# Kernel optimization log

Measured on AMD Instinct MI355X. Metric: run time of the kernel, lower is better.

Reference implementation:

```python
import jax, jax.numpy as jnp
import numpy as np

ROPE_THETA = 500000.0


def apply_rope(x, position_ids):
    # x: (B, H, S, hd), position_ids: (B, S)
    hd = x.shape[-1]
    inv_freq = 1.0 / (ROPE_THETA ** (jnp.arange(0, hd, 2, dtype=x.dtype) / hd))  # (hd/2,)
    freqs = position_ids.astype(x.dtype)[:, :, None] * inv_freq  # (B, S, hd/2)
    sin = jnp.sin(freqs)[:, None, :, :]  # (B, 1, S, hd/2)
    cos = jnp.cos(freqs)[:, None, :, :]
    x1 = x[..., ::2]
    x2 = x[..., 1::2]
    even = x1 * cos - x2 * sin
    odd = x2 * cos + x1 * sin
    # interleave even/odd back: stack on a new trailing axis then flatten
    return jnp.stack([even, odd], axis=-1).reshape(x.shape)


def setup_inputs() -> dict:
    key = jax.random.key(0)
    k_x, k_q, k_k, k_v, k_o = jax.random.split(key, 5)
    B, S, D = 2, 2048, 2048
    H, H_kv = 32, 8
    hd = D // H
    x = jax.random.normal(k_x, (B, S, D), dtype=jnp.float32)
    position_ids = jnp.broadcast_to(jnp.arange(S, dtype=jnp.int64)[None, :], (B, S))
    scale = 0.02
    Wq = jax.random.normal(k_q, (D, H * hd), dtype=jnp.float32) * scale
    Wk = jax.random.normal(k_k, (D, H_kv * hd), dtype=jnp.float32) * scale
    Wv = jax.random.normal(k_v, (D, H_kv * hd), dtype=jnp.float32) * scale
    Wo = jax.random.normal(k_o, (D, D), dtype=jnp.float32) * scale
    return {"x": x, "position_ids": position_ids, "Wq": Wq, "Wk": Wk, "Wv": Wv, "Wo": Wo}


def reference(x, position_ids, Wq, Wk, Wv, Wo):
    B, S, D = x.shape
    H, H_kv = 32, 8
    hd = D // H
    G = H // H_kv  # query heads per kv head

    q = (x @ Wq).reshape(B, S, H, hd).transpose(0, 2, 1, 3)        # (B, H, S, hd)
    k = (x @ Wk).reshape(B, S, H_kv, hd).transpose(0, 2, 1, 3)     # (B, H_kv, S, hd)
    v = (x @ Wv).reshape(B, S, H_kv, hd).transpose(0, 2, 1, 3)

    q = apply_rope(q, position_ids)
    k = apply_rope(k, position_ids)

    # GQA: group query heads (B, H_kv, G, S, hd); repeat_interleave maps head h -> kv head h // G
    qg = q.reshape(B, H_kv, G, S, hd)
    scores = jnp.einsum("bkgsh,bkth->bkgst", qg, k) / jnp.sqrt(jnp.asarray(hd, x.dtype))

    causal = jnp.triu(jnp.ones((S, S), dtype=bool), 1)  # True = masked
    scores = jnp.where(causal, jnp.asarray(-jnp.inf, scores.dtype), scores)

    attn = jax.nn.softmax(scores, axis=-1)  # (B, H_kv, G, S, S)
    z = jnp.einsum("bkgst,bkth->bkgsh", attn, v)  # (B, H_kv, G, S, hd)
    z = z.reshape(B, H, S, hd).transpose(0, 2, 1, 3).reshape(B, S, D)
    return z @ Wo
```

## Files before the change

kernel.cpp:

```cpp
#include <hip/hip_runtime.h>
#include <hip/hip_bf16.h>


#define S_LEN 2048
#define DIM   2048
#define NH    32
#define NKV   8
#define HD    64
#define BS    4096
#define NQKV  3072
#define LL(x) ((long long)(x))

typedef __bf16 bf16x8 __attribute__((ext_vector_type(8)));
typedef float  f32x4  __attribute__((ext_vector_type(4)));
typedef float  f32x16 __attribute__((ext_vector_type(16)));
typedef unsigned u32x4 __attribute__((ext_vector_type(4)));

__device__ __forceinline__ unsigned short bfb(float f) {
  __hip_bfloat16 h = __float2bfloat16(f);
  return *reinterpret_cast<unsigned short*>(&h);
}

__device__ __forceinline__ unsigned cvtpk(float lo, float hi) {
  unsigned u;
  asm("v_cvt_pk_bf16_f32 %0, %1, %2" : "=v"(u) : "v"(lo), "v"(hi));
  return u;
}

__device__ __forceinline__ void gload16(const void* g, void* l) {
  __builtin_amdgcn_global_load_lds(
      (const __attribute__((address_space(1))) void*)g,
      (__attribute__((address_space(3))) void*)l, 16, 0, 0);
}

__device__ __forceinline__ void tcast_body(
    const float* __restrict__ in, unsigned short* __restrict__ out,
    int K, int N, int bx, int by, int tid, float* tile ) {
  int n0 = bx * 32, k0 = by * 32;
  int tx = tid & 31, ty = tid >> 5;
#pragma unroll
  for (int r = 0; r < 32; r += 8)
    tile[(ty + r) * 33 + tx] = in[LL(k0 + ty + r) * N + n0 + tx];
  __syncthreads();
#pragma unroll
  for (int r = 0; r < 32; r += 8)
    out[LL(n0 + ty + r) * K + k0 + tx] = bfb(tile[tx * 33 + ty + r]);
}

__global__ __launch_bounds__(256) void k_prep(
    const float* __restrict__ x,  const float* __restrict__ Wq,
    const float* __restrict__ Wk, const float* __restrict__ Wv,
    const float* __restrict__ Wo, float* __restrict__ tab,
    unsigned short* __restrict__ xb, unsigned short* __restrict__ wqkvt,
    unsigned short* __restrict__ wot) {
  __shared__ float tile[32 * 33];
  int blk = blockIdx.x, tid = threadIdx.x;
  if (blk < 256) {
    int i = blk * 256 + tid;
    int s = i >> 5, f = i & 31;
    double inv = pow(500000.0, -2.0 * (double)f / 64.0);
    double fr = (double)s * inv;
    tab[2 * i]     = (float)cos(fr);
    tab[2 * i + 1] = (float)sin(fr);
  } else if (blk < 8448) {
    int i = (blk - 256) * 256 + tid;
    float4 v = ((const float4*)x)[i];
    ushort4 o;
    o.x = bfb(v.x); o.y = bfb(v.y); o.z = bfb(v.z); o.w = bfb(v.w);
    ((ushort4*)xb)[i] = o;
  } else if (blk < 12544) {
    int t2 = blk - 8448;
    tcast_body(Wq, wqkvt, DIM, DIM, t2 & 63, t2 >> 6, tid, tile);
  } else if (blk < 13568) {
    int t3 = blk - 12544;
    tcast_body(Wk, wqkvt + LL(2048) * DIM, DIM, 512, t3 & 15, t3 >> 4, tid, tile);
  } else if (blk < 14592) {
    int t4 = blk - 13568;
    tcast_body(Wv, wqkvt + LL(2560) * DIM, DIM, 512, t4 & 15, t4 >> 4, tid, tile);
  } else {
    int t5 = blk - 14592;
    tcast_body(Wo, wot, DIM, DIM, t5 & 63, t5 >> 6, tid, tile);
  }
}

template <int MODE>
__global__ __launch_bounds__(256, 2) void k_gemm(
    const unsigned short* __restrict__ A, const unsigned short* __restrict__ Bt,
    void* __restrict__ Cout, int M, int N, int K,
    const float* __restrict__ tab, unsigned short* __restrict__ qbuf,
    unsigned short* __restrict__ kbuf, unsigned short* __restrict__ vtb) {
  __shared__ __align__(16) unsigned short As[128 * 64];
  __shared__ __align__(16) unsigned short Bs[128 * 64];
  int t = threadIdx.x;
  int lane = t & 63, w = t >> 6;
  int wr = w >> 1, wc = w & 1;
  int g = lane >> 4, r = lane & 15;
  int sw = (r & 7) * 8;
  int gx = gridDim.x;
  int nwg = gx * gridDim.y;
  int lin = blockIdx.y * gx + blockIdx.x;
  int cpx = nwg >> 3;
  int swz = (lin & 7) * cpx + (lin >> 3);
  int bx = swz % gx, by = swz / gx;
  long long rowBase = LL(by) * 128;
  long long colBase = LL(bx) * 128;

  f32x4 acc[4][4] = {};

  int c0 = t, c1 = t + 256, c2 = t + 512, c3 = t + 768;
#define SRCP(P, base, c) ((P) + ((base) + ((c) >> 3)) * K \
                               + ((((c) & 7) ^ (((c) >> 3) & 7)) * 8))
  const unsigned short* ag0 = SRCP(A, rowBase, c0);
  const unsigned short* ag1 = SRCP(A, rowBase, c1);
  const unsigned short* ag2 = SRCP(A, rowBase, c2);
  const unsigned short* ag3 = SRCP(A, rowBase, c3);
  const unsigned short* bg0 = SRCP(Bt, colBase, c0);
  const unsigned short* bg1 = SRCP(Bt, colBase, c1);
  const unsigned short* bg2 = SRCP(Bt, colBase, c2);
  const unsigned short* bg3 = SRCP(Bt, colBase, c3);
#undef SRCP
  char* lA0 = (char*)As + c0 * 16; char* lA1 = (char*)As + c1 * 16;
  char* lA2 = (char*)As + c2 * 16; char* lA3 = (char*)As + c3 * 16;
  char* lB0 = (char*)Bs + c0 * 16; char* lB1 = (char*)Bs + c1 * 16;
  char* lB2 = (char*)Bs + c2 * 16; char* lB3 = (char*)Bs + c3 * 16;

  for (int kt = 0; kt < K; kt += 64) {
    __syncthreads();
    gload16(ag0 + kt, lA0);
    gload16(ag1 + kt, lA1);
    gload16(ag2 + kt, lA2);
    gload16(ag3 + kt, lA3);
    gload16(bg0 + kt, lB0);
    gload16(bg1 + kt, lB1);
    gload16(bg2 + kt, lB2);
    gload16(bg3 + kt, lB3);
    __syncthreads();

#pragma unroll
    for (int kd = 0; kd < 2; kd++) {
      bf16x8 af[4], bfr[4];
#pragma unroll
      for (int m = 0; m < 4; m++)
        af[m] = *(const bf16x8*)(const void*)(
            As + (wr * 64 + m * 16 + r) * 64 + ((kd * 32 + g * 8) ^ sw));
#pragma unroll
      for (int n = 0; n < 4; n++)
        bfr[n] = *(const bf16x8*)(const void*)(
            Bs + (wc * 64 + n * 16 + r) * 64 + ((kd * 32 + g * 8) ^ sw));
#pragma unroll
      for (int m = 0; m < 4; m++)
#pragma unroll
        for (int n = 0; n < 4; n++)
          acc[m][n] = __builtin_amdgcn_mfma_f32_16x16x32_bf16(af[m], bfr[n], acc[m][n], 0, 0, 0);
    }
  }

  if (MODE == 0) {
#pragma unroll
    for (int m = 0; m < 4; m++)
#pragma unroll
      for (int n = 0; n < 4; n++) {
        long long row0 = rowBase + wr * 64 + m * 16 + g * 4;
        long long col = colBase + wc * 64 + n * 16 + r;
#pragma unroll
        for (int j = 0; j < 4; j++)
          ((float*)Cout)[(row0 + j) * N + col] = acc[m][n][j];
      }
  } else {
#pragma unroll
    for (int n = 0; n < 4; n++) {
      int gc0 = (int)colBase + wc * 64 + n * 16;
      int gc = gc0 + r;
      if (gc0 < 2560) {
        unsigned short* dst; int dcol, dstride; float scale;
        if (gc0 < 2048) { dst = qbuf; dcol = gc;        dstride = DIM; scale = 0.18033688f; }
        else            { dst = kbuf; dcol = gc - 2048; dstride = 512; scale = 1.0f; }
        int f = (gc & 63) >> 1;
        float sgn = (gc & 1) ? 1.f : -1.f;
#pragma unroll
        for (int m = 0; m < 4; m++) {
          long long row0 = rowBase + wr * 64 + m * 16 + g * 4;
#pragma unroll
          for (int j = 0; j < 4; j++) {
            float v = acc[m][n][j];
            float part = __shfl_xor(v, 1);
            int s = (int)((row0 + j) & (S_LEN - 1));
            float cc = tab[(s * 32 + f) * 2], ss = tab[(s * 32 + f) * 2 + 1];
            float o = (v * cc + sgn * part * ss) * scale;
            dst[(row0 + j) * dstride + dcol] = bfb(o);
          }
        }
      } else {
        int dcol = gc - 2560;
#pragma unroll
        for (int m = 0; m < 4; m++) {
          long long row0 = rowBase + wr * 64 + m * 16 + g * 4;
#pragma unroll
          for (int j = 0; j < 4; j++) {
            long long row = row0 + j;
            long long bq = row >> 11;
            int s = (int)(row & (S_LEN - 1));
            vtb[(bq * 512 + dcol) * S_LEN + s] = bfb(acc[m][n][j]);
          }
        }
      }
    }
  }
}

__global__ __launch_bounds__(256, 2) void k_attn(
    const unsigned short* __restrict__ qb, const unsigned short* __restrict__ kb,
    const unsigned short* __restrict__ vt, unsigned short* __restrict__ zb) {
  int lin = blockIdx.x + 16 * (blockIdx.y + 32 * blockIdx.z);
  int kvh = lin & 7;
  int idx = lin >> 3;
  int st = 15 - (idx >> 3);
  int b = (idx >> 2) & 1;
  int h = kvh * 4 + (idx & 3);
  int bh = b * NKV + kvh;

  int t = threadIdx.x, lane = t & 63, w = t >> 6;
  int l31 = lane & 31, hi = lane >> 5;
  int sw = (l31 & 7) * 8;

  __shared__ __align__(16) unsigned short Ks[2][64 * 64];
  __shared__ __align__(16) unsigned short Vs[2][64 * 64];

  int c0 = t, c1 = t + 256;
  const unsigned short* kg0 = kb + LL(b) * S_LEN * 512 + (c0 >> 3) * 512 + kvh * HD
                                 + (((c0 & 7) ^ ((c0 >> 3) & 7)) * 8);
  const unsigned short* kg1 = kb + LL(b) * S_LEN * 512 + (c1 >> 3) * 512 + kvh * HD
                                 + (((c1 & 7) ^ ((c1 >> 3) & 7)) * 8);
  const unsigned short* vg0 = vt + (LL(bh) * HD + (c0 >> 3)) * S_LEN
                                 + (((c0 & 7) ^ ((c0 >> 3) & 7)) * 8);
  const unsigned short* vg1 = vt + (LL(bh) * HD + (c1 >> 3)) * S_LEN
                                 + (((c1 & 7) ^ ((c1 >> 3) & 7)) * 8);

#define STAGE(bufi, kst_)                                              \
  {                                                                    \
    gload16(kg0 + LL(kst_) * 512, (char*)Ks[bufi] + c0 * 16);          \
    gload16(kg1 + LL(kst_) * 512, (char*)Ks[bufi] + c1 * 16);          \
    gload16(vg0 + (kst_), (char*)Vs[bufi] + c0 * 16);                  \
    gload16(vg1 + (kst_), (char*)Vs[bufi] + c1 * 16);                  \
  }

  int rowb = st * 128 + w * 32;
  int qg = rowb + l31;
  long long qrow = LL(b) * S_LEN + qg;

  bf16x8 qf[4];
#pragma unroll
  for (int s = 0; s < 4; s++)
    qf[s] = *(const bf16x8*)(const void*)(qb + qrow * DIM + h * HD + s * 16 + hi * 8);

  f32x16 acc0 = {}, acc1 = {};
  float mrun = -1e30f, lrun = 0.f;

  int nt = 2 * st + 2;
  STAGE(0, 0);
  for (int tt = 0; tt < nt; tt++) {
    int kst = tt * 64;
    int cur = tt & 1;
    asm volatile("s_waitcnt vmcnt(0)" ::: "memory");
    __builtin_amdgcn_s_barrier();
    __builtin_amdgcn_sched_barrier(0);
    if (tt + 1 < nt) STAGE(cur ^ 1, kst + 64);

    if (kst <= rowb + 31) {
      const unsigned short* Kc = Ks[cur];
      const unsigned short* Vc = Vs[cur];

      bf16x8 kf[2][4];
#pragma unroll
      for (int kbi = 0; kbi < 2; kbi++)
#pragma unroll
        for (int s = 0; s < 4; s++)
          kf[kbi][s] = *(const bf16x8*)(const void*)(
              Kc + (kbi * 32 + l31) * 64 + ((s * 16 + hi * 8) ^ sw));

      __builtin_amdgcn_s_setprio(1);
      f32x16 sc0 = {}, sc1 = {};
#pragma unroll
      for (int s = 0; s < 4; s++) {
        sc0 = __builtin_amdgcn_mfma_f32_32x32x16_bf16(kf[0][s], qf[s], sc0, 0, 0, 0);
        sc1 = __builtin_amdgcn_mfma_f32_32x32x16_bf16(kf[1][s], qf[s], sc1, 0, 0, 0);
      }
      __builtin_amdgcn_s_setprio(0);

      bf16x8 vf[8];
#pragma unroll
      for (int db = 0; db < 2; db++)
#pragma unroll
        for (int f = 0; f < 4; f++)
          vf[db * 4 + f] = *(const bf16x8*)(const void*)(
              Vc + (db * 32 + l31) * 64 + ((f * 16 + hi * 8) ^ sw));

      if (kst + 63 > rowb) {
#pragma unroll
        for (int q = 0; q < 16; q++) {
          int kl = (q & 3) + 8 * (q >> 2) + 4 * hi;
          if (kst + kl > qg) sc0[q] = -1e30f;
          if (kst + 32 + kl > qg) sc1[q] = -1e30f;
        }
      }

      float pm = -1e30f;
#pragma unroll
      for (int q = 0; q < 16; q++) {
        pm = fmaxf(pm, sc0[q]);
        pm = fmaxf(pm, sc1[q]);
      }
      pm = fmaxf(pm, __shfl_xor(pm, 32));
      if (__any(pm > mrun + 12.0f)) {
        float mnew = fmaxf(mrun, pm);
        float al = exp2f(mrun - mnew);
        mrun = mnew;
        lrun *= al;
        acc0 *= al;
        acc1 *= al;
      }
      f32x16 pv0, pv1;
      float ls = 0.f;
#pragma unroll
      for (int q = 0; q < 16; q++) {
        pv0[q] = exp2f(sc0[q] - mrun);
        pv1[q] = exp2f(sc1[q] - mrun);
        ls += pv0[q] + pv1[q];
      }
      lrun += ls + __shfl_xor(ls, 32);

      bf16x8 pfr[4];
#pragma unroll
      for (int f = 0; f < 4; f++) {
        int qb_ = (f & 1) * 8;
        float e0, e1, e2, e3, e4, e5, e6, e7;
        if (f < 2) {
          e0 = pv0[qb_ + 0]; e1 = pv0[qb_ + 1]; e2 = pv0[qb_ + 2]; e3 = pv0[qb_ + 3];
          e4 = pv0[qb_ + 4]; e5 = pv0[qb_ + 5]; e6 = pv0[qb_ + 6]; e7 = pv0[qb_ + 7];
        } else {
          e0 = pv1[qb_ + 0]; e1 = pv1[qb_ + 1]; e2 = pv1[qb_ + 2]; e3 = pv1[qb_ + 3];
          e4 = pv1[qb_ + 4]; e5 = pv1[qb_ + 5]; e6 = pv1[qb_ + 6]; e7 = pv1[qb_ + 7];
        }
        unsigned a0 = cvtpk(e0, e1), a1 = cvtpk(e2, e3);
        unsigned b0 = cvtpk(e4, e5), b1 = cvtpk(e6, e7);
        asm volatile("v_permlane32_swap_b32 %0, %1" : "+v"(a0), "+v"(b0));
        asm volatile("v_permlane32_swap_b32 %0, %1" : "+v"(a1), "+v"(b1));
        u32x4 uu;
        uu[0] = a0;
        uu[1] = a1;
        uu[2] = b0;
        uu[3] = b1;
        pfr[f] = *(bf16x8*)&uu;
      }

      __builtin_amdgcn_s_setprio(1);
#pragma unroll
      for (int f = 0; f < 4; f++) {
        acc0 = __builtin_amdgcn_mfma_f32_32x32x16_bf16(vf[f],     pfr[f], acc0, 0, 0, 0);
        acc1 = __builtin_amdgcn_mfma_f32_32x32x16_bf16(vf[4 + f], pfr[f], acc1, 0, 0, 0);
      }
      __builtin_amdgcn_s_setprio(0);
    }
  }

  float invl = 1.0f / lrun;
#pragma unroll
  for (int q4 = 0; q4 < 4; q4++) {
    uint2 u;
    u.x = cvtpk(acc0[q4 * 4 + 0] * invl, acc0[q4 * 4 + 1] * invl);
    u.y = cvtpk(acc0[q4 * 4 + 2] * invl, acc0[q4 * 4 + 3] * invl);
    *(uint2*)(void*)(zb + qrow * DIM + h * HD + 8 * q4 + 4 * hi) = u;
    uint2 v;
    v.x = cvtpk(acc1[q4 * 4 + 0] * invl, acc1[q4 * 4 + 1] * invl);
    v.y = cvtpk(acc1[q4 * 4 + 2] * invl, acc1[q4 * 4 + 3] * invl);
    *(uint2*)(void*)(zb + qrow * DIM + h * HD + 32 + 8 * q4 + 4 * hi) = v;
  }
#undef STAGE
}

extern "C" void kernel_launch(void* const* d_in, const int* in_sizes, int n_in,
                              void* d_out, int out_size, void* d_ws, size_t ws_size,
                              hipStream_t stream) {
  const float* x  = (const float*)d_in[0];
  const float* Wq = (const float*)d_in[2];
  const float* Wk = (const float*)d_in[3];
  const float* Wv = (const float*)d_in[4];
  const float* Wo = (const float*)d_in[5];
  float* out = (float*)d_out;

  char* wsb = (char*)d_ws;
  size_t off = 0;
  auto alloc = [&](size_t bytes) {
    void* p = wsb + off;
    off += (bytes + 255) & ~(size_t)255;
    return p;
  };
  float* tab            = (float*)alloc(LL(S_LEN) * 32 * 2 * 4);
  unsigned short* xb    = (unsigned short*)alloc(LL(BS) * DIM * 2);
  unsigned short* wqkvt = (unsigned short*)alloc(LL(NQKV) * DIM * 2);
  unsigned short* wot   = (unsigned short*)alloc(LL(DIM) * DIM * 2);
  unsigned short* qbuf  = (unsigned short*)alloc(LL(BS) * DIM * 2);
  unsigned short* kbuf  = (unsigned short*)alloc(LL(BS) * (NKV * HD) * 2);
  unsigned short* vtb   = (unsigned short*)alloc(LL(2 * NKV) * HD * S_LEN * 2);
  unsigned short* zb    = (unsigned short*)alloc(LL(BS) * DIM * 2);

  k_prep<<<18688, 256, 0, stream>>>(x, Wq, Wk, Wv, Wo, tab, xb, wqkvt, wot);

  k_gemm<2><<<dim3(NQKV / 128, BS / 128), 256, 0, stream>>>(
      xb, wqkvt, nullptr, BS, NQKV, DIM, tab, qbuf, kbuf, vtb);

  k_attn<<<dim3(16, NH, 2), 256, 0, stream>>>(qbuf, kbuf, vtb, zb);

  k_gemm<0><<<dim3(DIM / 128, BS / 128), 256, 0, stream>>>(
      zb, wot, out, BS, DIM, DIM, nullptr, nullptr, nullptr, nullptr);
}
```

Measured before the change: 187.9 us.

## Double-buffer LDS tiles in GEMM to overlap global loads with MFMA

The GEMM kernel now keeps two LDS buffers for the A and B tiles. It issues the global-to-LDS loads for the next K-tile right after the barrier, so they run while MFMAs consume the current tile. This replaces the old load, sync, compute sequence that serialized memory latency with compute. LDS use doubles to 64KB per block, which may limit the two-blocks-per-CU occupancy. The single barrier per iteration relies on the wait at the top of the loop to protect the buffer being reused.

```diff
diff --git a/kernel.cpp b/kernel.cpp
--- a/kernel.cpp
+++ b/kernel.cpp
@@ -89,8 +89,8 @@
     void* __restrict__ Cout, int M, int N, int K,
     const float* __restrict__ tab, unsigned short* __restrict__ qbuf,
     unsigned short* __restrict__ kbuf, unsigned short* __restrict__ vtb) {
-  __shared__ __align__(16) unsigned short As[128 * 64];
-  __shared__ __align__(16) unsigned short Bs[128 * 64];
+  __shared__ __align__(16) unsigned short As[2][128 * 64];
+  __shared__ __align__(16) unsigned short Bs[2][128 * 64];
   int t = threadIdx.x;
   int lane = t & 63, w = t >> 6;
   int wr = w >> 1, wc = w & 1;
@@ -119,34 +119,41 @@
   const unsigned short* bg2 = SRCP(Bt, colBase, c2);
   const unsigned short* bg3 = SRCP(Bt, colBase, c3);
 #undef SRCP
-  char* lA0 = (char*)As + c0 * 16; char* lA1 = (char*)As + c1 * 16;
-  char* lA2 = (char*)As + c2 * 16; char* lA3 = (char*)As + c3 * 16;
-  char* lB0 = (char*)Bs + c0 * 16; char* lB1 = (char*)Bs + c1 * 16;
-  char* lB2 = (char*)Bs + c2 * 16; char* lB3 = (char*)Bs + c3 * 16;
-
-  for (int kt = 0; kt < K; kt += 64) {
-    __syncthreads();
-    gload16(ag0 + kt, lA0);
-    gload16(ag1 + kt, lA1);
-    gload16(ag2 + kt, lA2);
-    gload16(ag3 + kt, lA3);
-    gload16(bg0 + kt, lB0);
-    gload16(bg1 + kt, lB1);
-    gload16(bg2 + kt, lB2);
-    gload16(bg3 + kt, lB3);
-    __syncthreads();
-
+
+#define GSTAGE(bufi, kt_)                                   \
+  {                                                         \
+    gload16(ag0 + (kt_), (char*)As[bufi] + c0 * 16);        \
+    gload16(ag1 + (kt_), (char*)As[bufi] + c1 * 16);        \
+    gload16(ag2 + (kt_), (char*)As[bufi] + c2 * 16);        \
+    gload16(ag3 + (kt_), (char*)As[bufi] + c3 * 16);        \
+    gload16(bg0 + (kt_), (char*)Bs[bufi] + c0 * 16);        \
+    gload16(bg1 + (kt_), (char*)Bs[bufi] + c1 * 16);        \
+    gload16(bg2 + (kt_), (char*)Bs[bufi] + c2 * 16);        \
+    gload16(bg3 + (kt_), (char*)Bs[bufi] + c3 * 16);        \
+  }
+
+  int nit = K >> 6;
+  GSTAGE(0, 0);
+  for (int it = 0; it < nit; it++) {
+    int cur = it & 1;
+    asm volatile("s_waitcnt vmcnt(0)" ::: "memory");
+    __builtin_amdgcn_s_barrier();
+    __builtin_amdgcn_sched_barrier(0);
+    if (it + 1 < nit) GSTAGE(cur ^ 1, (it + 1) * 64);
+
+    const unsigned short* Ac = As[cur];
+    const unsigned short* Bc = Bs[cur];
 #pragma unroll
     for (int kd = 0; kd < 2; kd++) {
       bf16x8 af[4], bfr[4];
 #pragma unroll
       for (int m = 0; m < 4; m++)
         af[m] = *(const bf16x8*)(const void*)(
-            As + (wr * 64 + m * 16 + r) * 64 + ((kd * 32 + g * 8) ^ sw));
+            Ac + (wr * 64 + m * 16 + r) * 64 + ((kd * 32 + g * 8) ^ sw));
 #pragma unroll
       for (int n = 0; n < 4; n++)
         bfr[n] = *(const bf16x8*)(const void*)(
-            Bs + (wc * 64 + n * 16 + r) * 64 + ((kd * 32 + g * 8) ^ sw));
+            Bc + (wc * 64 + n * 16 + r) * 64 + ((kd * 32 + g * 8) ^ sw));
 #pragma unroll
       for (int m = 0; m < 4; m++)
 #pragma unroll
@@ -154,6 +161,7 @@
           acc[m][n] = __builtin_amdgcn_mfma_f32_16x16x32_bf16(af[m], bfr[n], acc[m][n], 0, 0, 0);
     }
   }
+#undef GSTAGE
 
   if (MODE == 0) {
 #pragma unroll
```

After: 194.3 us. 3.4% more time.
